# Optimization experiments

Hardware: AMD Instinct MI355X
Metric: run time of the kernel (lower is better)

Reference implementation:

```python
import jax, jax.numpy as jnp
import numpy as np
import math

B, N, C = 4096, 64, 128
H = 4
HD = C // H


def setup_inputs() -> dict:
    key = jax.random.key(0)
    ks = jax.random.split(key, 8)
    s = 1.0 / math.sqrt(C)
    return {
        "x": jax.random.normal(ks[0], (B, N, C), dtype=jnp.float32),
        "entropy_map": jax.random.uniform(ks[1], (B, 1, N), dtype=jnp.float32),
        "Wq": jax.random.normal(ks[2], (C, C), dtype=jnp.float32) * s,
        "bq": jnp.zeros((C,), dtype=jnp.float32),
        "Wk": jax.random.normal(ks[3], (C, C), dtype=jnp.float32) * s,
        "bk": jnp.zeros((C,), dtype=jnp.float32),
        "Wv": jax.random.normal(ks[4], (C, C), dtype=jnp.float32) * s,
        "bv": jnp.zeros((C,), dtype=jnp.float32),
        "Wo": jax.random.normal(ks[5], (C, C), dtype=jnp.float32) * s,
        "bo": jnp.zeros((C,), dtype=jnp.float32),
        "beta": 1,
    }


def reference(x, entropy_map, Wq, bq, Wk, bk, Wv, bv, Wo, bo, beta):
    b, n, c = x.shape
    # torch Linear: y = x @ W^T + b
    def proj(w, bias):
        y = jnp.einsum("bnc,dc->bnd", x, w) + bias
        return y.reshape(b, n, H, HD).transpose(0, 2, 1, 3)  # (B,H,N,HD)

    Q = proj(Wq, bq)
    K = proj(Wk, bk)
    V = proj(Wv, bv)
    scale = 1.0 / math.sqrt(HD)
    scores = jnp.einsum("bhnd,bhmd->bhnm", Q, K) * scale  # (B,H,N,N)
    attn = jax.nn.softmax(scores, axis=-1)
    # entropy gating: (B,1,N) -> (B,1,1,N), scales key columns then renormalizes
    gating = jnp.exp(-beta * entropy_map)[:, None, :, :]
    attn = attn * gating
    attn = attn / (attn.sum(axis=-1, keepdims=True) + 1e-9)
    out = jnp.einsum("bhnm,bhmd->bhnd", attn, V)  # (B,H,N,HD)
    out = out.transpose(0, 2, 1, 3).reshape(b, n, c)
    return jnp.einsum("bnc,dc->bnd", out, Wo) + bo
```

## Files before the change

### kernel.cpp

```cpp
#include <hip/hip_runtime.h>
#include <hip/hip_bf16.h>

#define NTOK 64
#define CDIM 128

typedef __attribute__((ext_vector_type(4))) float  f32x4;
typedef __attribute__((ext_vector_type(8))) short  bf16x8;
typedef __attribute__((ext_vector_type(4))) short  s16x4;

__device__ __forceinline__ s16x4 pk4(f32x4 v) {
  union { __hip_bfloat162 h[2]; s16x4 s; } u;
  u.h[0] = __float22bfloat162_rn(float2{v.x, v.y});
  u.h[1] = __float22bfloat162_rn(float2{v.z, v.w});
  return u.s;
}

__device__ __forceinline__ int swz(int row, int cb, int stride) {
  return row * stride + (cb ^ ((row & 7) << 4));
}

__global__ void wconv_kernel(const float* __restrict__ wq, const float* __restrict__ wk,
                             const float* __restrict__ wv, const float* __restrict__ wo,
                             short* __restrict__ wbf) {
  int t = (blockIdx.x * 256 + threadIdx.x) * 4;
  f32x4 a = *reinterpret_cast<const f32x4*>(wq + t);
  f32x4 b = *reinterpret_cast<const f32x4*>(wk + t);
  f32x4 c = *reinterpret_cast<const f32x4*>(wv + t);
  f32x4 d = *reinterpret_cast<const f32x4*>(wo + t);
  *reinterpret_cast<s16x4*>(wbf + t)         = pk4(a);
  *reinterpret_cast<s16x4*>(wbf + 16384 + t) = pk4(b);
  *reinterpret_cast<s16x4*>(wbf + 32768 + t) = pk4(c);
  *reinterpret_cast<s16x4*>(wbf + 49152 + t) = pk4(d);
}

#define A_OFF    0
#define B_OFF    16384
#define C_OFF    32768
#define GATE_OFF 49152
#define SMEM_BYTES (49152 + 256)

__global__ __launch_bounds__(256, 3) void fused_attn(
    const float* __restrict__ x, const float* __restrict__ ent,
    const short* __restrict__ wbf,
    const float* __restrict__ bq, const float* __restrict__ bk,
    const float* __restrict__ bv, const float* __restrict__ bo,
    const int* __restrict__ beta, float* __restrict__ out)
{
  __shared__ unsigned char sm[SMEM_BYTES];
  float* gate = (float*)(sm + GATE_OFF);
  const int tid  = threadIdx.x;
  const int lane = tid & 63;
  const int w    = tid >> 6;
  const int g    = lane >> 4;
  const int li   = lane & 15;
  const int b    = blockIdx.x;

  {
    const float* xb = x + (size_t)b * (NTOK * CDIM);
    #pragma unroll
    for (int it = 0; it < 8; ++it) {
      int f = (tid + 256 * it) * 4;
      int row = f >> 7, col = f & 127;
      f32x4 v = *reinterpret_cast<const f32x4*>(xb + f);
      *reinterpret_cast<s16x4*>(sm + A_OFF + swz(row, col * 2, 256)) = pk4(v);
    }
    if (tid < NTOK) gate[tid] = -(float)beta[0] * ent[(size_t)b * NTOK + tid];
  }
  __syncthreads();

  bf16x8 xf[4][4];
  #pragma unroll
  for (int ti = 0; ti < 4; ++ti)
    #pragma unroll
    for (int kk = 0; kk < 4; ++kk)
      xf[ti][kk] = *reinterpret_cast<const bf16x8*>(sm + A_OFF + swz(ti * 16 + li, (kk * 32 + g * 8) * 2, 256));

  __syncthreads();

  const f32x4 zero4 = {0.f, 0.f, 0.f, 0.f};

  {
    const short* wv_ = wbf + 32768;
    f32x4 accv[4][2];
    #pragma unroll
    for (int mi = 0; mi < 4; ++mi) { accv[mi][0] = zero4; accv[mi][1] = zero4; }
    bf16x8 bfv[2][4];
    #pragma unroll
    for (int n2 = 0; n2 < 2; ++n2)
      #pragma unroll
      for (int kk = 0; kk < 4; ++kk)
        bfv[n2][kk] = *reinterpret_cast<const bf16x8*>(wv_ + (w * 32 + n2 * 16 + li) * CDIM + kk * 32 + g * 8);
    #pragma unroll
    for (int mi = 0; mi < 4; ++mi)
      #pragma unroll
      for (int n2 = 0; n2 < 2; ++n2)
        #pragma unroll
        for (int kk = 0; kk < 4; ++kk)
          accv[mi][n2] = __builtin_amdgcn_mfma_f32_16x16x32_bf16(xf[mi][kk], bfv[n2][kk], accv[mi][n2], 0, 0, 0);
    #pragma unroll
    for (int mi = 0; mi < 4; ++mi)
      #pragma unroll
      for (int n2 = 0; n2 < 2; ++n2) {
        int d = w * 32 + n2 * 16 + li;
        float bb = bv[d];
        f32x4 v = accv[mi][n2];
        v.x += bb; v.y += bb; v.z += bb; v.w += bb;
        *reinterpret_cast<s16x4*>(sm + C_OFF + swz(d, (mi * 16 + g * 4) * 2, 128)) = pk4(v);
      }
  }

  {
    const short* wmat = wbf + ((w < 2) ? 0 : 16384);
    const float* bias = (w < 2) ? bq : bk;
    const int dbase   = (w & 1) * 64;
    const int qkoff   = (w < 2) ? A_OFF : B_OFF;

    #pragma unroll
    for (int mi = 0; mi < 4; ++mi) {
      bf16x8 af[4];
      #pragma unroll
      for (int kk = 0; kk < 4; ++kk)
        af[kk] = *reinterpret_cast<const bf16x8*>(wmat + (dbase + mi * 16 + li) * CDIM + kk * 32 + g * 8);
      f32x4 acc[4];
      #pragma unroll
      for (int ni = 0; ni < 4; ++ni) acc[ni] = zero4;
      #pragma unroll
      for (int ni = 0; ni < 4; ++ni)
        #pragma unroll
        for (int kk = 0; kk < 4; ++kk)
          acc[ni] = __builtin_amdgcn_mfma_f32_16x16x32_bf16(af[kk], xf[ni][kk], acc[ni], 0, 0, 0);
      int d0 = dbase + mi * 16 + g * 4;
      float4 b4 = *reinterpret_cast<const float4*>(bias + d0);
      #pragma unroll
      for (int ni = 0; ni < 4; ++ni) {
        f32x4 v = acc[ni];
        v.x += b4.x; v.y += b4.y; v.z += b4.z; v.w += b4.w;
        *reinterpret_cast<s16x4*>(sm + qkoff + swz(ni * 16 + li, d0 * 2, 256)) = pk4(v);
      }
    }
  }
  __syncthreads();

  const float scale = 0.17677669529663688f;
  f32x4 st[4][4];
  {
    bf16x8 kf[4], qf[4];
    int cb = (w * 32 + g * 8) * 2;
    #pragma unroll
    for (int t = 0; t < 4; ++t) {
      kf[t] = *reinterpret_cast<const bf16x8*>(sm + B_OFF + swz(t * 16 + li, cb, 256));
      qf[t] = *reinterpret_cast<const bf16x8*>(sm + A_OFF + swz(t * 16 + li, cb, 256));
    }
    #pragma unroll
    for (int mj = 0; mj < 4; ++mj)
      #pragma unroll
      for (int ni = 0; ni < 4; ++ni)
        st[mj][ni] = __builtin_amdgcn_mfma_f32_16x16x32_bf16(kf[mj], qf[ni], zero4, 0, 0, 0);
  }
  float gv[16];
  #pragma unroll
  for (int mj = 0; mj < 4; ++mj)
    #pragma unroll
    for (int r = 0; r < 4; ++r)
      gv[mj * 4 + r] = gate[mj * 16 + g * 4 + r];

  #pragma unroll
  for (int ni = 0; ni < 4; ++ni) {
    float mx = -3.0e38f;
    #pragma unroll
    for (int mj = 0; mj < 4; ++mj) {
      f32x4 v = st[mj][ni];
      v.x = v.x * scale + gv[mj * 4 + 0];
      v.y = v.y * scale + gv[mj * 4 + 1];
      v.z = v.z * scale + gv[mj * 4 + 2];
      v.w = v.w * scale + gv[mj * 4 + 3];
      st[mj][ni] = v;
      mx = fmaxf(mx, fmaxf(fmaxf(v.x, v.y), fmaxf(v.z, v.w)));
    }
    mx = fmaxf(mx, __shfl_xor(mx, 16));
    mx = fmaxf(mx, __shfl_xor(mx, 32));
    float sum = 0.f;
    #pragma unroll
    for (int mj = 0; mj < 4; ++mj) {
      f32x4 v = st[mj][ni];
      v.x = __expf(v.x - mx); v.y = __expf(v.y - mx);
      v.z = __expf(v.z - mx); v.w = __expf(v.w - mx);
      st[mj][ni] = v;
      sum += v.x + v.y + v.z + v.w;
    }
    sum += __shfl_xor(sum, 16);
    sum += __shfl_xor(sum, 32);
    float inv = 1.f / (sum + 1e-9f);
    #pragma unroll
    for (int mj = 0; mj < 4; ++mj) {
      st[mj][ni].x *= inv; st[mj][ni].y *= inv;
      st[mj][ni].z *= inv; st[mj][ni].w *= inv;
    }
  }
  __syncthreads();

  unsigned char* pb = sm + w * 8192;
  #pragma unroll
  for (int mj = 0; mj < 4; ++mj) {
    int cb = (mj * 16 + g * 4) * 2;
    #pragma unroll
    for (int ni = 0; ni < 4; ++ni)
      *reinterpret_cast<s16x4*>(pb + swz(ni * 16 + li, cb, 128)) = pk4(st[mj][ni]);
  }

  {
    f32x4 accO[2][4];
    #pragma unroll
    for (int md = 0; md < 2; ++md)
      #pragma unroll
      for (int ni = 0; ni < 4; ++ni) accO[md][ni] = zero4;
    bf16x8 vf[2][2];
    #pragma unroll
    for (int md = 0; md < 2; ++md)
      #pragma unroll
      for (int ks = 0; ks < 2; ++ks)
        vf[md][ks] = *reinterpret_cast<const bf16x8*>(sm + C_OFF + swz(w * 32 + md * 16 + li, (ks * 32 + g * 8) * 2, 128));
    bf16x8 pf[4][2];
    #pragma unroll
    for (int ni = 0; ni < 4; ++ni)
      #pragma unroll
      for (int ks = 0; ks < 2; ++ks)
        pf[ni][ks] = *reinterpret_cast<const bf16x8*>(pb + swz(ni * 16 + li, (ks * 32 + g * 8) * 2, 128));
    #pragma unroll
    for (int md = 0; md < 2; ++md)
      #pragma unroll
      for (int ni = 0; ni < 4; ++ni)
        #pragma unroll
        for (int ks = 0; ks < 2; ++ks)
          accO[md][ni] = __builtin_amdgcn_mfma_f32_16x16x32_bf16(vf[md][ks], pf[ni][ks], accO[md][ni], 0, 0, 0);
    __syncthreads();
    #pragma unroll
    for (int md = 0; md < 2; ++md) {
      int cb = (w * 32 + md * 16 + g * 4) * 2;
      #pragma unroll
      for (int ni = 0; ni < 4; ++ni)
        *reinterpret_cast<s16x4*>(sm + C_OFF + swz(ni * 16 + li, cb, 256)) = pk4(accO[md][ni]);
    }
  }
  __syncthreads();

  {
    const short* wo_ = wbf + 49152;
    f32x4 accY[2][4];
    #pragma unroll
    for (int mi = 0; mi < 2; ++mi)
      #pragma unroll
      for (int ni = 0; ni < 4; ++ni) accY[mi][ni] = zero4;
    bf16x8 wfa[2][4];
    #pragma unroll
    for (int mi = 0; mi < 2; ++mi)
      #pragma unroll
      for (int kk = 0; kk < 4; ++kk)
        wfa[mi][kk] = *reinterpret_cast<const bf16x8*>(wo_ + (w * 32 + mi * 16 + li) * CDIM + kk * 32 + g * 8);
    bf16x8 of[4][4];
    #pragma unroll
    for (int ni = 0; ni < 4; ++ni)
      #pragma unroll
      for (int kk = 0; kk < 4; ++kk)
        of[ni][kk] = *reinterpret_cast<const bf16x8*>(sm + C_OFF + swz(ni * 16 + li, (kk * 32 + g * 8) * 2, 256));
    #pragma unroll
    for (int mi = 0; mi < 2; ++mi)
      #pragma unroll
      for (int ni = 0; ni < 4; ++ni)
        #pragma unroll
        for (int kk = 0; kk < 4; ++kk)
          accY[mi][ni] = __builtin_amdgcn_mfma_f32_16x16x32_bf16(wfa[mi][kk], of[ni][kk], accY[mi][ni], 0, 0, 0);
    float* yb = out + (size_t)b * (NTOK * CDIM);
    #pragma unroll
    for (int mi = 0; mi < 2; ++mi) {
      int dout0 = w * 32 + mi * 16 + g * 4;
      float4 bo4 = *reinterpret_cast<const float4*>(bo + dout0);
      #pragma unroll
      for (int ni = 0; ni < 4; ++ni) {
        int i = ni * 16 + li;
        f32x4 y = accY[mi][ni];
        y.x += bo4.x; y.y += bo4.y; y.z += bo4.z; y.w += bo4.w;
        *reinterpret_cast<f32x4*>(yb + i * CDIM + dout0) = y;
      }
    }
  }
}

extern "C" void kernel_launch(void* const* d_in, const int* in_sizes, int n_in,
                              void* d_out, int out_size, void* d_ws, size_t ws_size,
                              hipStream_t stream) {
  const float* x    = (const float*)d_in[0];
  const float* ent  = (const float*)d_in[1];
  const float* wq   = (const float*)d_in[2];
  const float* bq   = (const float*)d_in[3];
  const float* wk   = (const float*)d_in[4];
  const float* bk   = (const float*)d_in[5];
  const float* wv   = (const float*)d_in[6];
  const float* bv   = (const float*)d_in[7];
  const float* wo   = (const float*)d_in[8];
  const float* bo   = (const float*)d_in[9];
  const int*   beta = (const int*)d_in[10];

  short* wbf = (short*)d_ws;
  const int B = in_sizes[0] / (NTOK * CDIM);

  wconv_kernel<<<16, 256, 0, stream>>>(wq, wk, wv, wo, wbf);
  fused_attn<<<B, 256, 0, stream>>>(x, ent, wbf, bq, bk, bv, bo, beta, (float*)d_out);
}
```

Baseline: 99.86 us.

## Shrink shared memory to 32KB, drop softmax max, fold scale into Wq

Cuts shared memory from about 48KB to 32KB by keeping the V projection in registers and staging V^T and P in two halves through the reused Q/K buffers. The launch-bounds occupancy hint rises from 3 to 4 blocks per CU. The attention scale is folded into Wq and bq at weight-conversion time, and the softmax max-subtraction is removed because the rows renormalise anyway. The gate is now read straight from global memory. This trades extra barriers and register pressure for occupancy, and dropping the max is only safe while the scores stay small enough that exp does not overflow.

Result: slower. 154.7 us (+54.9%).

```diff
diff --git a/kernel.cpp b/kernel.cpp
--- a/kernel.cpp
+++ b/kernel.cpp
@@ -3,6 +3,7 @@
 
 #define NTOK 64
 #define CDIM 128
+#define SCALE 0.17677669529663688f
 
 typedef __attribute__((ext_vector_type(4))) float  f32x4;
 typedef __attribute__((ext_vector_type(8))) short  bf16x8;
@@ -18,12 +19,16 @@
 __device__ __forceinline__ int swz(int row, int cb, int stride) {
   return row * stride + (cb ^ ((row & 7) << 4));
 }
+__device__ __forceinline__ int swz64(int row, int cb) {
+  return row * 64 + (cb ^ ((row & 3) << 4));
+}
 
 __global__ void wconv_kernel(const float* __restrict__ wq, const float* __restrict__ wk,
                              const float* __restrict__ wv, const float* __restrict__ wo,
                              short* __restrict__ wbf) {
   int t = (blockIdx.x * 256 + threadIdx.x) * 4;
   f32x4 a = *reinterpret_cast<const f32x4*>(wq + t);
+  a.x *= SCALE; a.y *= SCALE; a.z *= SCALE; a.w *= SCALE;
   f32x4 b = *reinterpret_cast<const f32x4*>(wk + t);
   f32x4 c = *reinterpret_cast<const f32x4*>(wv + t);
   f32x4 d = *reinterpret_cast<const f32x4*>(wo + t);
@@ -33,13 +38,11 @@
   *reinterpret_cast<s16x4*>(wbf + 49152 + t) = pk4(d);
 }
 
-#define A_OFF    0
-#define B_OFF    16384
-#define C_OFF    32768
-#define GATE_OFF 49152
-#define SMEM_BYTES (49152 + 256)
-
-__global__ __launch_bounds__(256, 3) void fused_attn(
+#define A_OFF 0
+#define B_OFF 16384
+#define SMEM_BYTES 32768
+
+__global__ __launch_bounds__(256, 4) void fused_attn(
     const float* __restrict__ x, const float* __restrict__ ent,
     const short* __restrict__ wbf,
     const float* __restrict__ bq, const float* __restrict__ bk,
@@ -47,7 +50,6 @@
     const int* __restrict__ beta, float* __restrict__ out)
 {
   __shared__ unsigned char sm[SMEM_BYTES];
-  float* gate = (float*)(sm + GATE_OFF);
   const int tid  = threadIdx.x;
   const int lane = tid & 63;
   const int w    = tid >> 6;
@@ -64,7 +66,6 @@
       f32x4 v = *reinterpret_cast<const f32x4*>(xb + f);
       *reinterpret_cast<s16x4*>(sm + A_OFF + swz(row, col * 2, 256)) = pk4(v);
     }
-    if (tid < NTOK) gate[tid] = -(float)beta[0] * ent[(size_t)b * NTOK + tid];
   }
   __syncthreads();
 
@@ -79,6 +80,7 @@
 
   const f32x4 zero4 = {0.f, 0.f, 0.f, 0.f};
 
+  s16x4 vtpk[4][2];
   {
     const short* wv_ = wbf + 32768;
     f32x4 accv[4][2];
@@ -101,17 +103,17 @@
     for (int mi = 0; mi < 4; ++mi)
       #pragma unroll
       for (int n2 = 0; n2 < 2; ++n2) {
-        int d = w * 32 + n2 * 16 + li;
-        float bb = bv[d];
+        float bb = bv[w * 32 + n2 * 16 + li];
         f32x4 v = accv[mi][n2];
         v.x += bb; v.y += bb; v.z += bb; v.w += bb;
-        *reinterpret_cast<s16x4*>(sm + C_OFF + swz(d, (mi * 16 + g * 4) * 2, 128)) = pk4(v);
+        vtpk[mi][n2] = pk4(v);
       }
   }
 
   {
     const short* wmat = wbf + ((w < 2) ? 0 : 16384);
     const float* bias = (w < 2) ? bq : bk;
+    const float bsc   = (w < 2) ? SCALE : 1.0f;
     const int dbase   = (w & 1) * 64;
     const int qkoff   = (w < 2) ? A_OFF : B_OFF;
 
@@ -131,6 +133,7 @@
           acc[ni] = __builtin_amdgcn_mfma_f32_16x16x32_bf16(af[kk], xf[ni][kk], acc[ni], 0, 0, 0);
       int d0 = dbase + mi * 16 + g * 4;
       float4 b4 = *reinterpret_cast<const float4*>(bias + d0);
+      b4.x *= bsc; b4.y *= bsc; b4.z *= bsc; b4.w *= bsc;
       #pragma unroll
       for (int ni = 0; ni < 4; ++ni) {
         f32x4 v = acc[ni];
@@ -141,7 +144,6 @@
   }
   __syncthreads();
 
-  const float scale = 0.17677669529663688f;
   f32x4 st[4][4];
   {
     bf16x8 kf[4], qf[4];
@@ -157,34 +159,25 @@
       for (int ni = 0; ni < 4; ++ni)
         st[mj][ni] = __builtin_amdgcn_mfma_f32_16x16x32_bf16(kf[mj], qf[ni], zero4, 0, 0, 0);
   }
-  float gv[16];
-  #pragma unroll
-  for (int mj = 0; mj < 4; ++mj)
-    #pragma unroll
-    for (int r = 0; r < 4; ++r)
-      gv[mj * 4 + r] = gate[mj * 16 + g * 4 + r];
+  float4 gv[4];
+  {
+    const float nb = -(float)beta[0];
+    const float* eb = ent + (size_t)b * NTOK;
+    #pragma unroll
+    for (int mj = 0; mj < 4; ++mj) {
+      float4 e = *reinterpret_cast<const float4*>(eb + mj * 16 + g * 4);
+      gv[mj].x = nb * e.x; gv[mj].y = nb * e.y; gv[mj].z = nb * e.z; gv[mj].w = nb * e.w;
+    }
+  }
 
   #pragma unroll
   for (int ni = 0; ni < 4; ++ni) {
-    float mx = -3.0e38f;
+    float sum = 0.f;
     #pragma unroll
     for (int mj = 0; mj < 4; ++mj) {
       f32x4 v = st[mj][ni];
-      v.x = v.x * scale + gv[mj * 4 + 0];
-      v.y = v.y * scale + gv[mj * 4 + 1];
-      v.z = v.z * scale + gv[mj * 4 + 2];
-      v.w = v.w * scale + gv[mj * 4 + 3];
-      st[mj][ni] = v;
-      mx = fmaxf(mx, fmaxf(fmaxf(v.x, v.y), fmaxf(v.z, v.w)));
-    }
-    mx = fmaxf(mx, __shfl_xor(mx, 16));
-    mx = fmaxf(mx, __shfl_xor(mx, 32));
-    float sum = 0.f;
-    #pragma unroll
-    for (int mj = 0; mj < 4; ++mj) {
-      f32x4 v = st[mj][ni];
-      v.x = __expf(v.x - mx); v.y = __expf(v.y - mx);
-      v.z = __expf(v.z - mx); v.w = __expf(v.w - mx);
+      v.x = __expf(v.x + gv[mj].x); v.y = __expf(v.y + gv[mj].y);
+      v.z = __expf(v.z + gv[mj].z); v.w = __expf(v.w + gv[mj].w);
       st[mj][ni] = v;
       sum += v.x + v.y + v.z + v.w;
     }
@@ -199,48 +192,72 @@
   }
   __syncthreads();
 
-  unsigned char* pb = sm + w * 8192;
-  #pragma unroll
-  for (int mj = 0; mj < 4; ++mj) {
-    int cb = (mj * 16 + g * 4) * 2;
-    #pragma unroll
-    for (int ni = 0; ni < 4; ++ni)
-      *reinterpret_cast<s16x4*>(pb + swz(ni * 16 + li, cb, 128)) = pk4(st[mj][ni]);
-  }
-
-  {
-    f32x4 accO[2][4];
+  unsigned char* vtb = sm + B_OFF + w * 4096;
+  unsigned char* pbb = sm + A_OFF + w * 4096;
+
+  #pragma unroll
+  for (int mi = 0; mi < 4; ++mi)
+    #pragma unroll
+    for (int n2 = 0; n2 < 2; ++n2)
+      *reinterpret_cast<s16x4*>(vtb + swz(n2 * 16 + li, (mi * 16 + g * 4) * 2, 128)) = vtpk[mi][n2];
+  #pragma unroll
+  for (int mjp = 0; mjp < 2; ++mjp)
+    #pragma unroll
+    for (int ni = 0; ni < 4; ++ni)
+      *reinterpret_cast<s16x4*>(pbb + swz64(ni * 16 + li, (mjp * 16 + g * 4) * 2)) = pk4(st[mjp][ni]);
+  __syncthreads();
+
+  f32x4 accO[2][4];
+  #pragma unroll
+  for (int md = 0; md < 2; ++md)
+    #pragma unroll
+    for (int ni = 0; ni < 4; ++ni) accO[md][ni] = zero4;
+
+  {
+    bf16x8 vf[2], pf[4];
     #pragma unroll
     for (int md = 0; md < 2; ++md)
-      #pragma unroll
-      for (int ni = 0; ni < 4; ++ni) accO[md][ni] = zero4;
-    bf16x8 vf[2][2];
+      vf[md] = *reinterpret_cast<const bf16x8*>(vtb + swz(md * 16 + li, (g * 8) * 2, 128));
+    #pragma unroll
+    for (int ni = 0; ni < 4; ++ni)
+      pf[ni] = *reinterpret_cast<const bf16x8*>(pbb + swz64(ni * 16 + li, g * 16));
     #pragma unroll
     for (int md = 0; md < 2; ++md)
       #pragma unroll
-      for (int ks = 0; ks < 2; ++ks)
-        vf[md][ks] = *reinterpret_cast<const bf16x8*>(sm + C_OFF + swz(w * 32 + md * 16 + li, (ks * 32 + g * 8) * 2, 128));
-    bf16x8 pf[4][2];
-    #pragma unroll
-    for (int ni = 0; ni < 4; ++ni)
-      #pragma unroll
-      for (int ks = 0; ks < 2; ++ks)
-        pf[ni][ks] = *reinterpret_cast<const bf16x8*>(pb + swz(ni * 16 + li, (ks * 32 + g * 8) * 2, 128));
+      for (int ni = 0; ni < 4; ++ni)
+        accO[md][ni] = __builtin_amdgcn_mfma_f32_16x16x32_bf16(vf[md], pf[ni], accO[md][ni], 0, 0, 0);
+  }
+  __syncthreads();
+
+  #pragma unroll
+  for (int mjp = 0; mjp < 2; ++mjp)
+    #pragma unroll
+    for (int ni = 0; ni < 4; ++ni)
+      *reinterpret_cast<s16x4*>(pbb + swz64(ni * 16 + li, (mjp * 16 + g * 4) * 2)) = pk4(st[2 + mjp][ni]);
+  __syncthreads();
+
+  {
+    bf16x8 vf[2], pf[4];
     #pragma unroll
     for (int md = 0; md < 2; ++md)
-      #pragma unroll
-      for (int ni = 0; ni < 4; ++ni)
-        #pragma unroll
-        for (int ks = 0; ks < 2; ++ks)
-          accO[md][ni] = __builtin_amdgcn_mfma_f32_16x16x32_bf16(vf[md][ks], pf[ni][ks], accO[md][ni], 0, 0, 0);
-    __syncthreads();
-    #pragma unroll
-    for (int md = 0; md < 2; ++md) {
-      int cb = (w * 32 + md * 16 + g * 4) * 2;
-      #pragma unroll
-      for (int ni = 0; ni < 4; ++ni)
-        *reinterpret_cast<s16x4*>(sm + C_OFF + swz(ni * 16 + li, cb, 256)) = pk4(accO[md][ni]);
-    }
+      vf[md] = *reinterpret_cast<const bf16x8*>(vtb + swz(md * 16 + li, (32 + g * 8) * 2, 128));
+    #pragma unroll
+    for (int ni = 0; ni < 4; ++ni)
+      pf[ni] = *reinterpret_cast<const bf16x8*>(pbb + swz64(ni * 16 + li, g * 16));
+    #pragma unroll
+    for (int md = 0; md < 2; ++md)
+      #pragma unroll
+      for (int ni = 0; ni < 4; ++ni)
+        accO[md][ni] = __builtin_amdgcn_mfma_f32_16x16x32_bf16(vf[md], pf[ni], accO[md][ni], 0, 0, 0);
+  }
+  __syncthreads();
+
+  #pragma unroll
+  for (int md = 0; md < 2; ++md) {
+    int cb = (w * 32 + md * 16 + g * 4) * 2;
+    #pragma unroll
+    for (int ni = 0; ni < 4; ++ni)
+      *reinterpret_cast<s16x4*>(sm + A_OFF + swz(ni * 16 + li, cb, 256)) = pk4(accO[md][ni]);
   }
   __syncthreads();
 
@@ -262,7 +279,7 @@
     for (int ni = 0; ni < 4; ++ni)
       #pragma unroll
       for (int kk = 0; kk < 4; ++kk)
-        of[ni][kk] = *reinterpret_cast<const bf16x8*>(sm + C_OFF + swz(ni * 16 + li, (kk * 32 + g * 8) * 2, 256));
+        of[ni][kk] = *reinterpret_cast<const bf16x8*>(sm + A_OFF + swz(ni * 16 + li, (kk * 32 + g * 8) * 2, 256));
     #pragma unroll
     for (int mi = 0; mi < 2; ++mi)
       #pragma unroll
```

## Process two batches per block with prefetch of next x tile

Applied to the files above, without the earlier changes.

Each block now handles two batch elements, loading the second batch's x into registers during the first batch's compute and storing it to shared memory before the output projection. The softmax drops the max-subtraction and folds the attention scale into the Q projection, with gate values read straight from global memory instead of shared memory. This aims to hide global load latency and trim softmax work, at the cost of extra registers, half as many blocks, and a risk of overflow since the max is no longer subtracted. It also assumes B is even.

After: 171.5 us. +71.8%, slower.

```diff
diff --git a/kernel.cpp b/kernel.cpp
--- a/kernel.cpp
+++ b/kernel.cpp
@@ -3,6 +3,7 @@
 
 #define NTOK 64
 #define CDIM 128
+#define SCALE 0.17677669529663688f
 
 typedef __attribute__((ext_vector_type(4))) float  f32x4;
 typedef __attribute__((ext_vector_type(8))) short  bf16x8;
@@ -33,11 +34,10 @@
   *reinterpret_cast<s16x4*>(wbf + 49152 + t) = pk4(d);
 }
 
-#define A_OFF    0
-#define B_OFF    16384
-#define C_OFF    32768
-#define GATE_OFF 49152
-#define SMEM_BYTES (49152 + 256)
+#define A_OFF 0
+#define B_OFF 16384
+#define C_OFF 32768
+#define SMEM_BYTES 49152
 
 __global__ __launch_bounds__(256, 3) void fused_attn(
     const float* __restrict__ x, const float* __restrict__ ent,
@@ -47,193 +47,197 @@
     const int* __restrict__ beta, float* __restrict__ out)
 {
   __shared__ unsigned char sm[SMEM_BYTES];
-  float* gate = (float*)(sm + GATE_OFF);
   const int tid  = threadIdx.x;
   const int lane = tid & 63;
   const int w    = tid >> 6;
   const int g    = lane >> 4;
   const int li   = lane & 15;
-  const int b    = blockIdx.x;
+
+  const int b0 = blockIdx.x;
+  const int b1 = blockIdx.x + gridDim.x;
+
+  f32x4 xn[8];
 
   {
-    const float* xb = x + (size_t)b * (NTOK * CDIM);
-    #pragma unroll
-    for (int it = 0; it < 8; ++it) {
-      int f = (tid + 256 * it) * 4;
+    const float* xb = x + (size_t)b0 * (NTOK * CDIM);
+    #pragma unroll
+    for (int i = 0; i < 8; ++i) {
+      int f = (tid + 256 * i) * 4;
       int row = f >> 7, col = f & 127;
       f32x4 v = *reinterpret_cast<const f32x4*>(xb + f);
       *reinterpret_cast<s16x4*>(sm + A_OFF + swz(row, col * 2, 256)) = pk4(v);
     }
-    if (tid < NTOK) gate[tid] = -(float)beta[0] * ent[(size_t)b * NTOK + tid];
   }
   __syncthreads();
 
-  bf16x8 xf[4][4];
-  #pragma unroll
-  for (int ti = 0; ti < 4; ++ti)
-    #pragma unroll
-    for (int kk = 0; kk < 4; ++kk)
-      xf[ti][kk] = *reinterpret_cast<const bf16x8*>(sm + A_OFF + swz(ti * 16 + li, (kk * 32 + g * 8) * 2, 256));
-
-  __syncthreads();
-
   const f32x4 zero4 = {0.f, 0.f, 0.f, 0.f};
 
-  {
-    const short* wv_ = wbf + 32768;
-    f32x4 accv[4][2];
-    #pragma unroll
-    for (int mi = 0; mi < 4; ++mi) { accv[mi][0] = zero4; accv[mi][1] = zero4; }
-    bf16x8 bfv[2][4];
-    #pragma unroll
-    for (int n2 = 0; n2 < 2; ++n2)
+  #define LDA(t, kk) (*reinterpret_cast<const bf16x8*>( \
+      sm + A_OFF + swz((t) * 16 + li, ((kk) * 32 + g * 8) * 2, 256)))
+
+  auto run = [&](int bb, bool prefetch_next, int bnext) {
+    bf16x8 xf[4][4];
+    #pragma unroll
+    for (int ti = 0; ti < 4; ++ti)
       #pragma unroll
       for (int kk = 0; kk < 4; ++kk)
-        bfv[n2][kk] = *reinterpret_cast<const bf16x8*>(wv_ + (w * 32 + n2 * 16 + li) * CDIM + kk * 32 + g * 8);
-    #pragma unroll
-    for (int mi = 0; mi < 4; ++mi)
+        xf[ti][kk] = LDA(ti, kk);
+    if (prefetch_next) {
+      const float* xb = x + (size_t)bnext * (NTOK * CDIM);
+      #pragma unroll
+      for (int i = 0; i < 8; ++i)
+        xn[i] = *reinterpret_cast<const f32x4*>(xb + (tid + 256 * i) * 4);
+    }
+    __syncthreads();
+
+    {
+      const short* wv_ = wbf + 32768;
+      f32x4 accv[4][2];
+      #pragma unroll
+      for (int mi = 0; mi < 4; ++mi) { accv[mi][0] = zero4; accv[mi][1] = zero4; }
+      bf16x8 bfv[2][4];
       #pragma unroll
       for (int n2 = 0; n2 < 2; ++n2)
         #pragma unroll
         for (int kk = 0; kk < 4; ++kk)
-          accv[mi][n2] = __builtin_amdgcn_mfma_f32_16x16x32_bf16(xf[mi][kk], bfv[n2][kk], accv[mi][n2], 0, 0, 0);
-    #pragma unroll
-    for (int mi = 0; mi < 4; ++mi)
-      #pragma unroll
-      for (int n2 = 0; n2 < 2; ++n2) {
-        int d = w * 32 + n2 * 16 + li;
-        float bb = bv[d];
-        f32x4 v = accv[mi][n2];
-        v.x += bb; v.y += bb; v.z += bb; v.w += bb;
-        *reinterpret_cast<s16x4*>(sm + C_OFF + swz(d, (mi * 16 + g * 4) * 2, 128)) = pk4(v);
-      }
-  }
-
-  {
-    const short* wmat = wbf + ((w < 2) ? 0 : 16384);
-    const float* bias = (w < 2) ? bq : bk;
-    const int dbase   = (w & 1) * 64;
-    const int qkoff   = (w < 2) ? A_OFF : B_OFF;
-
-    #pragma unroll
-    for (int mi = 0; mi < 4; ++mi) {
-      bf16x8 af[4];
-      #pragma unroll
-      for (int kk = 0; kk < 4; ++kk)
-        af[kk] = *reinterpret_cast<const bf16x8*>(wmat + (dbase + mi * 16 + li) * CDIM + kk * 32 + g * 8);
-      f32x4 acc[4];
-      #pragma unroll
-      for (int ni = 0; ni < 4; ++ni) acc[ni] = zero4;
+          bfv[n2][kk] = *reinterpret_cast<const bf16x8*>(wv_ + (w * 32 + n2 * 16 + li) * CDIM + kk * 32 + g * 8);
+      #pragma unroll
+      for (int mi = 0; mi < 4; ++mi)
+        #pragma unroll
+        for (int n2 = 0; n2 < 2; ++n2)
+          #pragma unroll
+          for (int kk = 0; kk < 4; ++kk)
+            accv[mi][n2] = __builtin_amdgcn_mfma_f32_16x16x32_bf16(xf[mi][kk], bfv[n2][kk], accv[mi][n2], 0, 0, 0);
+      #pragma unroll
+      for (int mi = 0; mi < 4; ++mi)
+        #pragma unroll
+        for (int n2 = 0; n2 < 2; ++n2) {
+          int d = w * 32 + n2 * 16 + li;
+          float bb_ = bv[d];
+          f32x4 v = accv[mi][n2];
+          v.x += bb_; v.y += bb_; v.z += bb_; v.w += bb_;
+          *reinterpret_cast<s16x4*>(sm + C_OFF + swz(d, (mi * 16 + g * 4) * 2, 128)) = pk4(v);
+        }
+    }
+
+    {
+      const short* wmat = wbf + ((w < 2) ? 0 : 16384);
+      const float* bias = (w < 2) ? bq : bk;
+      const float bsc   = (w < 2) ? SCALE : 1.0f;
+      const int dbase   = (w & 1) * 64;
+      const int qkoff   = (w < 2) ? A_OFF : B_OFF;
+      #pragma unroll
+      for (int mi = 0; mi < 4; ++mi) {
+        bf16x8 af[4];
+        #pragma unroll
+        for (int kk = 0; kk < 4; ++kk)
+          af[kk] = *reinterpret_cast<const bf16x8*>(wmat + (dbase + mi * 16 + li) * CDIM + kk * 32 + g * 8);
+        f32x4 acc[4];
+        #pragma unroll
+        for (int ni = 0; ni < 4; ++ni) acc[ni] = zero4;
+        #pragma unroll
+        for (int ni = 0; ni < 4; ++ni)
+          #pragma unroll
+          for (int kk = 0; kk < 4; ++kk)
+            acc[ni] = __builtin_amdgcn_mfma_f32_16x16x32_bf16(af[kk], xf[ni][kk], acc[ni], 0, 0, 0);
+        int d0 = dbase + mi * 16 + g * 4;
+        float4 b4 = *reinterpret_cast<const float4*>(bias + d0);
+        b4.x *= bsc; b4.y *= bsc; b4.z *= bsc; b4.w *= bsc;
+        #pragma unroll
+        for (int ni = 0; ni < 4; ++ni) {
+          f32x4 v = acc[ni];
+          v.x = v.x * bsc + b4.x; v.y = v.y * bsc + b4.y;
+          v.z = v.z * bsc + b4.z; v.w = v.w * bsc + b4.w;
+          *reinterpret_cast<s16x4*>(sm + qkoff + swz(ni * 16 + li, d0 * 2, 256)) = pk4(v);
+        }
+      }
+    }
+    __syncthreads();
+
+    f32x4 st[4][4];
+    {
+      bf16x8 kf[4], qf[4];
+      int cb = (w * 32 + g * 8) * 2;
+      #pragma unroll
+      for (int t = 0; t < 4; ++t) {
+        kf[t] = *reinterpret_cast<const bf16x8*>(sm + B_OFF + swz(t * 16 + li, cb, 256));
+        qf[t] = *reinterpret_cast<const bf16x8*>(sm + A_OFF + swz(t * 16 + li, cb, 256));
+      }
+      #pragma unroll
+      for (int mj = 0; mj < 4; ++mj)
+        #pragma unroll
+        for (int ni = 0; ni < 4; ++ni)
+          st[mj][ni] = __builtin_amdgcn_mfma_f32_16x16x32_bf16(kf[mj], qf[ni], zero4, 0, 0, 0);
+    }
+    float4 gv[4];
+    {
+      const float nb = -(float)beta[0];
+      const float* eb = ent + (size_t)bb * NTOK;
+      #pragma unroll
+      for (int mj = 0; mj < 4; ++mj) {
+        float4 e = *reinterpret_cast<const float4*>(eb + mj * 16 + g * 4);
+        gv[mj].x = nb * e.x; gv[mj].y = nb * e.y; gv[mj].z = nb * e.z; gv[mj].w = nb * e.w;
+      }
+    }
+    #pragma unroll
+    for (int ni = 0; ni < 4; ++ni) {
+      float sum = 0.f;
+      #pragma unroll
+      for (int mj = 0; mj < 4; ++mj) {
+        f32x4 v = st[mj][ni];
+        v.x = __expf(v.x + gv[mj].x); v.y = __expf(v.y + gv[mj].y);
+        v.z = __expf(v.z + gv[mj].z); v.w = __expf(v.w + gv[mj].w);
+        st[mj][ni] = v;
+        sum += v.x + v.y + v.z + v.w;
+      }
+      sum += __shfl_xor(sum, 16);
+      sum += __shfl_xor(sum, 32);
+      float inv = 1.f / (sum + 1e-9f);
+      #pragma unroll
+      for (int mj = 0; mj < 4; ++mj) {
+        st[mj][ni].x *= inv; st[mj][ni].y *= inv;
+        st[mj][ni].z *= inv; st[mj][ni].w *= inv;
+      }
+    }
+    __syncthreads();
+
+    unsigned char* pb = sm + w * 8192;
+    #pragma unroll
+    for (int mj = 0; mj < 4; ++mj) {
+      int cb = (mj * 16 + g * 4) * 2;
       #pragma unroll
       for (int ni = 0; ni < 4; ++ni)
-        #pragma unroll
-        for (int kk = 0; kk < 4; ++kk)
-          acc[ni] = __builtin_amdgcn_mfma_f32_16x16x32_bf16(af[kk], xf[ni][kk], acc[ni], 0, 0, 0);
-      int d0 = dbase + mi * 16 + g * 4;
-      float4 b4 = *reinterpret_cast<const float4*>(bias + d0);
-      #pragma unroll
-      for (int ni = 0; ni < 4; ++ni) {
-        f32x4 v = acc[ni];
-        v.x += b4.x; v.y += b4.y; v.z += b4.z; v.w += b4.w;
-        *reinterpret_cast<s16x4*>(sm + qkoff + swz(ni * 16 + li, d0 * 2, 256)) = pk4(v);
-      }
-    }
-  }
-  __syncthreads();
-
-  const float scale = 0.17677669529663688f;
-  f32x4 st[4][4];
-  {
-    bf16x8 kf[4], qf[4];
-    int cb = (w * 32 + g * 8) * 2;
-    #pragma unroll
-    for (int t = 0; t < 4; ++t) {
-      kf[t] = *reinterpret_cast<const bf16x8*>(sm + B_OFF + swz(t * 16 + li, cb, 256));
-      qf[t] = *reinterpret_cast<const bf16x8*>(sm + A_OFF + swz(t * 16 + li, cb, 256));
-    }
-    #pragma unroll
-    for (int mj = 0; mj < 4; ++mj)
+        *reinterpret_cast<s16x4*>(pb + swz(ni * 16 + li, cb, 128)) = pk4(st[mj][ni]);
+    }
+
+    f32x4 accO[2][4];
+    #pragma unroll
+    for (int md = 0; md < 2; ++md)
+      #pragma unroll
+      for (int ni = 0; ni < 4; ++ni) accO[md][ni] = zero4;
+    {
+      bf16x8 vf[2][2];
+      #pragma unroll
+      for (int md = 0; md < 2; ++md)
+        #pragma unroll
+        for (int ks = 0; ks < 2; ++ks)
+          vf[md][ks] = *reinterpret_cast<const bf16x8*>(sm + C_OFF + swz(w * 32 + md * 16 + li, (ks * 32 + g * 8) * 2, 128));
+      bf16x8 pf[4][2];
       #pragma unroll
       for (int ni = 0; ni < 4; ++ni)
-        st[mj][ni] = __builtin_amdgcn_mfma_f32_16x16x32_bf16(kf[mj], qf[ni], zero4, 0, 0, 0);
-  }
-  float gv[16];
-  #pragma unroll
-  for (int mj = 0; mj < 4; ++mj)
-    #pragma unroll
-    for (int r = 0; r < 4; ++r)
-      gv[mj * 4 + r] = gate[mj * 16 + g * 4 + r];
-
-  #pragma unroll
-  for (int ni = 0; ni < 4; ++ni) {
-    float mx = -3.0e38f;
-    #pragma unroll
-    for (int mj = 0; mj < 4; ++mj) {
-      f32x4 v = st[mj][ni];
-      v.x = v.x * scale + gv[mj * 4 + 0];
-      v.y = v.y * scale + gv[mj * 4 + 1];
-      v.z = v.z * scale + gv[mj * 4 + 2];
-      v.w = v.w * scale + gv[mj * 4 + 3];
-      st[mj][ni] = v;
-      mx = fmaxf(mx, fmaxf(fmaxf(v.x, v.y), fmaxf(v.z, v.w)));
-    }
-    mx = fmaxf(mx, __shfl_xor(mx, 16));
-    mx = fmaxf(mx, __shfl_xor(mx, 32));
-    float sum = 0.f;
-    #pragma unroll
-    for (int mj = 0; mj < 4; ++mj) {
-      f32x4 v = st[mj][ni];
-      v.x = __expf(v.x - mx); v.y = __expf(v.y - mx);
-      v.z = __expf(v.z - mx); v.w = __expf(v.w - mx);
-      st[mj][ni] = v;
-      sum += v.x + v.y + v.z + v.w;
-    }
-    sum += __shfl_xor(sum, 16);
-    sum += __shfl_xor(sum, 32);
-    float inv = 1.f / (sum + 1e-9f);
-    #pragma unroll
-    for (int mj = 0; mj < 4; ++mj) {
-      st[mj][ni].x *= inv; st[mj][ni].y *= inv;
-      st[mj][ni].z *= inv; st[mj][ni].w *= inv;
-    }
-  }
-  __syncthreads();
-
-  unsigned char* pb = sm + w * 8192;
-  #pragma unroll
-  for (int mj = 0; mj < 4; ++mj) {
-    int cb = (mj * 16 + g * 4) * 2;
-    #pragma unroll
-    for (int ni = 0; ni < 4; ++ni)
-      *reinterpret_cast<s16x4*>(pb + swz(ni * 16 + li, cb, 128)) = pk4(st[mj][ni]);
-  }
-
-  {
-    f32x4 accO[2][4];
-    #pragma unroll
-    for (int md = 0; md < 2; ++md)
-      #pragma unroll
-      for (int ni = 0; ni < 4; ++ni) accO[md][ni] = zero4;
-    bf16x8 vf[2][2];
-    #pragma unroll
-    for (int md = 0; md < 2; ++md)
-      #pragma unroll
-      for (int ks = 0; ks < 2; ++ks)
-        vf[md][ks] = *reinterpret_cast<const bf16x8*>(sm + C_OFF + swz(w * 32 + md * 16 + li, (ks * 32 + g * 8) * 2, 128));
-    bf16x8 pf[4][2];
-    #pragma unroll
-    for (int ni = 0; ni < 4; ++ni)
-      #pragma unroll
-      for (int ks = 0; ks < 2; ++ks)
-        pf[ni][ks] = *reinterpret_cast<const bf16x8*>(pb + swz(ni * 16 + li, (ks * 32 + g * 8) * 2, 128));
-    #pragma unroll
-    for (int md = 0; md < 2; ++md)
-      #pragma unroll
-      for (int ni = 0; ni < 4; ++ni)
         #pragma unroll
         for (int ks = 0; ks < 2; ++ks)
-          accO[md][ni] = __builtin_amdgcn_mfma_f32_16x16x32_bf16(vf[md][ks], pf[ni][ks], accO[md][ni], 0, 0, 0);
-    __syncthreads();
+          pf[ni][ks] = *reinterpret_cast<const bf16x8*>(pb + swz(ni * 16 + li, (ks * 32 + g * 8) * 2, 128));
+      #pragma unroll
+      for (int md = 0; md < 2; ++md)
+        #pragma unroll
+        for (int ni = 0; ni < 4; ++ni)
+          #pragma unroll
+          for (int ks = 0; ks < 2; ++ks)
+            accO[md][ni] = __builtin_amdgcn_mfma_f32_16x16x32_bf16(vf[md][ks], pf[ni][ks], accO[md][ni], 0, 0, 0);
+    }
+    __syncthreads();
+
     #pragma unroll
     for (int md = 0; md < 2; ++md) {
       int cb = (w * 32 + md * 16 + g * 4) * 2;
@@ -241,49 +245,57 @@
       for (int ni = 0; ni < 4; ++ni)
         *reinterpret_cast<s16x4*>(sm + C_OFF + swz(ni * 16 + li, cb, 256)) = pk4(accO[md][ni]);
     }
-  }
-  __syncthreads();
-
-  {
-    const short* wo_ = wbf + 49152;
-    f32x4 accY[2][4];
-    #pragma unroll
-    for (int mi = 0; mi < 2; ++mi)
-      #pragma unroll
-      for (int ni = 0; ni < 4; ++ni) accY[mi][ni] = zero4;
-    bf16x8 wfa[2][4];
-    #pragma unroll
-    for (int mi = 0; mi < 2; ++mi)
-      #pragma unroll
-      for (int kk = 0; kk < 4; ++kk)
-        wfa[mi][kk] = *reinterpret_cast<const bf16x8*>(wo_ + (w * 32 + mi * 16 + li) * CDIM + kk * 32 + g * 8);
-    bf16x8 of[4][4];
-    #pragma unroll
-    for (int ni = 0; ni < 4; ++ni)
-      #pragma unroll
-      for (int kk = 0; kk < 4; ++kk)
-        of[ni][kk] = *reinterpret_cast<const bf16x8*>(sm + C_OFF + swz(ni * 16 + li, (kk * 32 + g * 8) * 2, 256));
-    #pragma unroll
-    for (int mi = 0; mi < 2; ++mi)
+    if (prefetch_next) {
+      #pragma unroll
+      for (int i = 0; i < 8; ++i) {
+        int f = (tid + 256 * i) * 4;
+        int row = f >> 7, col = f & 127;
+        *reinterpret_cast<s16x4*>(sm + A_OFF + swz(row, col * 2, 256)) = pk4(xn[i]);
+      }
+    }
+    __syncthreads();
+
+    {
+      const short* wo_ = wbf + 49152;
+      f32x4 accY[2][4];
+      #pragma unroll
+      for (int mi = 0; mi < 2; ++mi)
+        #pragma unroll
+        for (int ni = 0; ni < 4; ++ni) accY[mi][ni] = zero4;
+      bf16x8 wfa[2][4];
+      #pragma unroll
+      for (int mi = 0; mi < 2; ++mi)
+        #pragma unroll
+        for (int kk = 0; kk < 4; ++kk)
+          wfa[mi][kk] = *reinterpret_cast<const bf16x8*>(wo_ + (w * 32 + mi * 16 + li) * CDIM + kk * 32 + g * 8);
       #pragma unroll
       for (int ni = 0; ni < 4; ++ni)
         #pragma unroll
-        for (int kk = 0; kk < 4; ++kk)
-          accY[mi][ni] = __builtin_amdgcn_mfma_f32_16x16x32_bf16(wfa[mi][kk], of[ni][kk], accY[mi][ni], 0, 0, 0);
-    float* yb = out + (size_t)b * (NTOK * CDIM);
-    #pragma unroll
-    for (int mi = 0; mi < 2; ++mi) {
-      int dout0 = w * 32 + mi * 16 + g * 4;
-      float4 bo4 = *reinterpret_cast<const float4*>(bo + dout0);
-      #pragma unroll
-      for (int ni = 0; ni < 4; ++ni) {
-        int i = ni * 16 + li;
-        f32x4 y = accY[mi][ni];
-        y.x += bo4.x; y.y += bo4.y; y.z += bo4.z; y.w += bo4.w;
-        *reinterpret_cast<f32x4*>(yb + i * CDIM + dout0) = y;
-      }
-    }
-  }
+        for (int kk = 0; kk < 4; ++kk) {
+          bf16x8 of = *reinterpret_cast<const bf16x8*>(sm + C_OFF + swz(ni * 16 + li, (kk * 32 + g * 8) * 2, 256));
+          accY[0][ni] = __builtin_amdgcn_mfma_f32_16x16x32_bf16(wfa[0][kk], of, accY[0][ni], 0, 0, 0);
+          accY[1][ni] = __builtin_amdgcn_mfma_f32_16x16x32_bf16(wfa[1][kk], of, accY[1][ni], 0, 0, 0);
+        }
+      float* yb = out + (size_t)bb * (NTOK * CDIM);
+      #pragma unroll
+      for (int mi = 0; mi < 2; ++mi) {
+        int dout0 = w * 32 + mi * 16 + g * 4;
+        float4 bo4 = *reinterpret_cast<const float4*>(bo + dout0);
+        #pragma unroll
+        for (int ni = 0; ni < 4; ++ni) {
+          int i = ni * 16 + li;
+          f32x4 y = accY[mi][ni];
+          y.x += bo4.x; y.y += bo4.y; y.z += bo4.z; y.w += bo4.w;
+          *reinterpret_cast<f32x4*>(yb + i * CDIM + dout0) = y;
+        }
+      }
+    }
+    __syncthreads();
+  };
+
+  run(b0, true, b1);
+  run(b1, false, 0);
+  #undef LDA
 }
 
 extern "C" void kernel_launch(void* const* d_in, const int* in_sizes, int n_in,
@@ -305,5 +317,5 @@
   const int B = in_sizes[0] / (NTOK * CDIM);
 
   wconv_kernel<<<16, 256, 0, stream>>>(wq, wk, wv, wo, wbf);
-  fused_attn<<<B, 256, 0, stream>>>(x, ent, wbf, bq, bk, bv, bo, beta, (float*)d_out);
-}
+  fused_attn<<<B / 2, 256, 0, stream>>>(x, ent, wbf, bq, bk, bv, bo, beta, (float*)d_out);
+}
```

## Fold softmax scale into Wq, drop max-subtraction, read gate directly, add setprio

Applied to the files above, without the earlier changes.

Pre-multiplies Wq and bq by the attention scale so scores need no scaling. Removes the row-max reduction and subtraction in softmax, which relies on scores being small enough not to overflow exp. Loads entropy gating values straight from global memory instead of staging them in LDS. Raises wave priority around the MFMA loops. The intent is to cut the ALU and shuffle work in softmax, at the cost of numerical robustness for large scores.

Result: slower. 107.7 us (+7.8%).

```diff
diff --git a/kernel.cpp b/kernel.cpp
--- a/kernel.cpp
+++ b/kernel.cpp
@@ -3,6 +3,7 @@
 
 #define NTOK 64
 #define CDIM 128
+#define SCALE 0.17677669529663688f
 
 typedef __attribute__((ext_vector_type(4))) float  f32x4;
 typedef __attribute__((ext_vector_type(8))) short  bf16x8;
@@ -24,6 +25,7 @@
                              short* __restrict__ wbf) {
   int t = (blockIdx.x * 256 + threadIdx.x) * 4;
   f32x4 a = *reinterpret_cast<const f32x4*>(wq + t);
+  a.x *= SCALE; a.y *= SCALE; a.z *= SCALE; a.w *= SCALE;
   f32x4 b = *reinterpret_cast<const f32x4*>(wk + t);
   f32x4 c = *reinterpret_cast<const f32x4*>(wv + t);
   f32x4 d = *reinterpret_cast<const f32x4*>(wo + t);
@@ -36,8 +38,7 @@
 #define A_OFF    0
 #define B_OFF    16384
 #define C_OFF    32768
-#define GATE_OFF 49152
-#define SMEM_BYTES (49152 + 256)
+#define SMEM_BYTES 49152
 
 __global__ __launch_bounds__(256, 3) void fused_attn(
     const float* __restrict__ x, const float* __restrict__ ent,
@@ -47,7 +48,6 @@
     const int* __restrict__ beta, float* __restrict__ out)
 {
   __shared__ unsigned char sm[SMEM_BYTES];
-  float* gate = (float*)(sm + GATE_OFF);
   const int tid  = threadIdx.x;
   const int lane = tid & 63;
   const int w    = tid >> 6;
@@ -64,7 +64,6 @@
       f32x4 v = *reinterpret_cast<const f32x4*>(xb + f);
       *reinterpret_cast<s16x4*>(sm + A_OFF + swz(row, col * 2, 256)) = pk4(v);
     }
-    if (tid < NTOK) gate[tid] = -(float)beta[0] * ent[(size_t)b * NTOK + tid];
   }
   __syncthreads();
 
@@ -90,6 +89,7 @@
       #pragma unroll
       for (int kk = 0; kk < 4; ++kk)
         bfv[n2][kk] = *reinterpret_cast<const bf16x8*>(wv_ + (w * 32 + n2 * 16 + li) * CDIM + kk * 32 + g * 8);
+    __builtin_amdgcn_s_setprio(1);
     #pragma unroll
     for (int mi = 0; mi < 4; ++mi)
       #pragma unroll
@@ -97,6 +97,7 @@
         #pragma unroll
         for (int kk = 0; kk < 4; ++kk)
           accv[mi][n2] = __builtin_amdgcn_mfma_f32_16x16x32_bf16(xf[mi][kk], bfv[n2][kk], accv[mi][n2], 0, 0, 0);
+    __builtin_amdgcn_s_setprio(0);
     #pragma unroll
     for (int mi = 0; mi < 4; ++mi)
       #pragma unroll
@@ -112,6 +113,7 @@
   {
     const short* wmat = wbf + ((w < 2) ? 0 : 16384);
     const float* bias = (w < 2) ? bq : bk;
+    const float bsc   = (w < 2) ? SCALE : 1.0f;
     const int dbase   = (w & 1) * 64;
     const int qkoff   = (w < 2) ? A_OFF : B_OFF;
 
@@ -124,13 +126,16 @@
       f32x4 acc[4];
       #pragma unroll
       for (int ni = 0; ni < 4; ++ni) acc[ni] = zero4;
+      __builtin_amdgcn_s_setprio(1);
       #pragma unroll
       for (int ni = 0; ni < 4; ++ni)
         #pragma unroll
         for (int kk = 0; kk < 4; ++kk)
           acc[ni] = __builtin_amdgcn_mfma_f32_16x16x32_bf16(af[kk], xf[ni][kk], acc[ni], 0, 0, 0);
+      __builtin_amdgcn_s_setprio(0);
       int d0 = dbase + mi * 16 + g * 4;
       float4 b4 = *reinterpret_cast<const float4*>(bias + d0);
+      b4.x *= bsc; b4.y *= bsc; b4.z *= bsc; b4.w *= bsc;
       #pragma unroll
       for (int ni = 0; ni < 4; ++ni) {
         f32x4 v = acc[ni];
@@ -141,7 +146,6 @@
   }
   __syncthreads();
 
-  const float scale = 0.17677669529663688f;
   f32x4 st[4][4];
   {
     bf16x8 kf[4], qf[4];
@@ -151,40 +155,33 @@
       kf[t] = *reinterpret_cast<const bf16x8*>(sm + B_OFF + swz(t * 16 + li, cb, 256));
       qf[t] = *reinterpret_cast<const bf16x8*>(sm + A_OFF + swz(t * 16 + li, cb, 256));
     }
+    __builtin_amdgcn_s_setprio(1);
     #pragma unroll
     for (int mj = 0; mj < 4; ++mj)
       #pragma unroll
       for (int ni = 0; ni < 4; ++ni)
         st[mj][ni] = __builtin_amdgcn_mfma_f32_16x16x32_bf16(kf[mj], qf[ni], zero4, 0, 0, 0);
-  }
-  float gv[16];
-  #pragma unroll
-  for (int mj = 0; mj < 4; ++mj)
-    #pragma unroll
-    for (int r = 0; r < 4; ++r)
-      gv[mj * 4 + r] = gate[mj * 16 + g * 4 + r];
+    __builtin_amdgcn_s_setprio(0);
+  }
+  float4 gv[4];
+  {
+    const float nb = -(float)beta[0];
+    const float* eb = ent + (size_t)b * NTOK;
+    #pragma unroll
+    for (int mj = 0; mj < 4; ++mj) {
+      float4 e = *reinterpret_cast<const float4*>(eb + mj * 16 + g * 4);
+      gv[mj].x = nb * e.x; gv[mj].y = nb * e.y; gv[mj].z = nb * e.z; gv[mj].w = nb * e.w;
+    }
+  }
 
   #pragma unroll
   for (int ni = 0; ni < 4; ++ni) {
-    float mx = -3.0e38f;
+    float sum = 0.f;
     #pragma unroll
     for (int mj = 0; mj < 4; ++mj) {
       f32x4 v = st[mj][ni];
-      v.x = v.x * scale + gv[mj * 4 + 0];
-      v.y = v.y * scale + gv[mj * 4 + 1];
-      v.z = v.z * scale + gv[mj * 4 + 2];
-      v.w = v.w * scale + gv[mj * 4 + 3];
-      st[mj][ni] = v;
-      mx = fmaxf(mx, fmaxf(fmaxf(v.x, v.y), fmaxf(v.z, v.w)));
-    }
-    mx = fmaxf(mx, __shfl_xor(mx, 16));
-    mx = fmaxf(mx, __shfl_xor(mx, 32));
-    float sum = 0.f;
-    #pragma unroll
-    for (int mj = 0; mj < 4; ++mj) {
-      f32x4 v = st[mj][ni];
-      v.x = __expf(v.x - mx); v.y = __expf(v.y - mx);
-      v.z = __expf(v.z - mx); v.w = __expf(v.w - mx);
+      v.x = __expf(v.x + gv[mj].x); v.y = __expf(v.y + gv[mj].y);
+      v.z = __expf(v.z + gv[mj].z); v.w = __expf(v.w + gv[mj].w);
       st[mj][ni] = v;
       sum += v.x + v.y + v.z + v.w;
     }
@@ -226,6 +223,7 @@
       #pragma unroll
       for (int ks = 0; ks < 2; ++ks)
         pf[ni][ks] = *reinterpret_cast<const bf16x8*>(pb + swz(ni * 16 + li, (ks * 32 + g * 8) * 2, 128));
+    __builtin_amdgcn_s_setprio(1);
     #pragma unroll
     for (int md = 0; md < 2; ++md)
       #pragma unroll
@@ -233,6 +231,7 @@
         #pragma unroll
         for (int ks = 0; ks < 2; ++ks)
           accO[md][ni] = __builtin_amdgcn_mfma_f32_16x16x32_bf16(vf[md][ks], pf[ni][ks], accO[md][ni], 0, 0, 0);
+    __builtin_amdgcn_s_setprio(0);
     __syncthreads();
     #pragma unroll
     for (int md = 0; md < 2; ++md) {
@@ -263,6 +262,7 @@
       #pragma unroll
       for (int kk = 0; kk < 4; ++kk)
         of[ni][kk] = *reinterpret_cast<const bf16x8*>(sm + C_OFF + swz(ni * 16 + li, (kk * 32 + g * 8) * 2, 256));
+    __builtin_amdgcn_s_setprio(1);
     #pragma unroll
     for (int mi = 0; mi < 2; ++mi)
       #pragma unroll
@@ -270,6 +270,7 @@
         #pragma unroll
         for (int kk = 0; kk < 4; ++kk)
           accY[mi][ni] = __builtin_amdgcn_mfma_f32_16x16x32_bf16(wfa[mi][kk], of[ni][kk], accY[mi][ni], 0, 0, 0);
+    __builtin_amdgcn_s_setprio(0);
     float* yb = out + (size_t)b * (NTOK * CDIM);
     #pragma unroll
     for (int mi = 0; mi < 2; ++mi) {
```
